# Optimization experiments

Hardware: AMD Instinct MI355X
Metric: run time of the kernel (lower is better)

Reference implementation:

```python
import jax, jax.numpy as jnp
import numpy as np

EPS = 1e-16  # matches PyG softmax denominator epsilon


def setup_inputs() -> dict:
    key = jax.random.key(0)
    k1, k2, k3, k4 = jax.random.split(key, 4)
    N, F, G = 200000, 256, 1024
    x = jax.random.normal(k1, (N, F), dtype=jnp.float32)
    batch = jnp.sort(jax.random.randint(k2, (N,), 0, G, dtype=jnp.int64))
    Wg = jax.random.normal(k3, (F, 1), dtype=jnp.float32) / np.sqrt(F)
    bg = jnp.zeros((1,), dtype=jnp.float32)
    Wn = jax.random.normal(k4, (F, F), dtype=jnp.float32) / np.sqrt(F)
    bn = jnp.zeros((F,), dtype=jnp.float32)
    return {"x": x, "batch": batch, "size": G, "Wg": Wg, "bg": bg, "Wn": Wn, "bn": bn}


def reference(x, batch, size, Wg, bg, Wn, bn):
    # gate scores: [N, 1]
    gate = x @ Wg + bg
    # transformed features: [N, F]
    h = x @ Wn + bn
    # per-graph (segment) softmax over gate, numerically stable
    seg_max = jax.ops.segment_max(gate, batch, num_segments=size)  # [G, 1]
    e = jnp.exp(gate - seg_max[batch])                             # [N, 1]
    seg_sum = jax.ops.segment_sum(e, batch, num_segments=size)     # [G, 1]
    alpha = e / (seg_sum[batch] + EPS)                             # [N, 1]
    # weighted scatter-add: [G, F]
    out = jax.ops.segment_sum(alpha * h, batch, num_segments=size)
    return out
```

## Files before the change

### kernel.cpp

```cpp
#include <hip/hip_runtime.h>
#include <math.h>

#define FDIM 256
#define EPSF 1e-16f
#define K4_ROWS 2

__device__ __forceinline__ float dot4(float4 a, float4 b) {
    return a.x * b.x + a.y * b.y + a.z * b.z + a.w * b.w;
}

__global__ void __launch_bounds__(256) k_ranges(const int* __restrict__ batch,
                                                int* __restrict__ seg_start,
                                                int N, int G) {
    int i = blockIdx.x * blockDim.x + threadIdx.x;
    if (i > N) return;
    int b  = (i == N) ? G : batch[i];
    int bp = (i == 0) ? -1 : batch[i - 1];
    for (int g = bp + 1; g <= b; ++g) seg_start[g] = i;
}

__global__ void __launch_bounds__(256) k_fused(const int* __restrict__ seg_start,
                                               const float* __restrict__ x,
                                               const float* __restrict__ Wg,
                                               float* __restrict__ yp,
                                               float* __restrict__ sp) {
    int b = blockIdx.x;
    int g = b >> 1, half = b & 1;
    int s0 = seg_start[g];
    int e0 = seg_start[g + 1];
    int mid = s0 + ((e0 - s0) >> 1);
    int rs = half ? mid : s0;
    int re = half ? e0 : mid;

    __shared__ float s_s[16];
    __shared__ float s_acc[16][FDIM];

    int wave = threadIdx.x >> 6;
    int group = (threadIdx.x >> 4) & 3;
    int l16 = threadIdx.x & 15;
    int part = (wave << 2) | group;

    const float4 wg0 = *reinterpret_cast<const float4*>(Wg +   0 + l16 * 4);
    const float4 wg1 = *reinterpret_cast<const float4*>(Wg +  64 + l16 * 4);
    const float4 wg2 = *reinterpret_cast<const float4*>(Wg + 128 + l16 * 4);
    const float4 wg3 = *reinterpret_cast<const float4*>(Wg + 192 + l16 * 4);

    float4 a0 = make_float4(0.f, 0.f, 0.f, 0.f);
    float4 a1 = a0, a2 = a0, a3 = a0;
    float s = 0.f;

    int r = rs + part;
    for (; r + 16 < re; r += 32) {
        const float* rp0 = x + (size_t)r * FDIM;
        const float* rp1 = x + (size_t)(r + 16) * FDIM;
        float4 x0 = *reinterpret_cast<const float4*>(rp0 +   0 + l16 * 4);
        float4 x1 = *reinterpret_cast<const float4*>(rp0 +  64 + l16 * 4);
        float4 x2 = *reinterpret_cast<const float4*>(rp0 + 128 + l16 * 4);
        float4 x3 = *reinterpret_cast<const float4*>(rp0 + 192 + l16 * 4);
        float4 y0 = *reinterpret_cast<const float4*>(rp1 +   0 + l16 * 4);
        float4 y1 = *reinterpret_cast<const float4*>(rp1 +  64 + l16 * 4);
        float4 y2 = *reinterpret_cast<const float4*>(rp1 + 128 + l16 * 4);
        float4 y3 = *reinterpret_cast<const float4*>(rp1 + 192 + l16 * 4);
        float d0 = dot4(x0, wg0) + dot4(x1, wg1) + dot4(x2, wg2) + dot4(x3, wg3);
        float d1 = dot4(y0, wg0) + dot4(y1, wg1) + dot4(y2, wg2) + dot4(y3, wg3);
        #pragma unroll
        for (int off = 1; off < 16; off <<= 1) {
            d0 += __shfl_xor(d0, off, 64);
            d1 += __shfl_xor(d1, off, 64);
        }
        float w0 = __expf(d0);
        float w1 = __expf(d1);
        a0.x += w0 * x0.x; a0.y += w0 * x0.y; a0.z += w0 * x0.z; a0.w += w0 * x0.w;
        a1.x += w0 * x1.x; a1.y += w0 * x1.y; a1.z += w0 * x1.z; a1.w += w0 * x1.w;
        a2.x += w0 * x2.x; a2.y += w0 * x2.y; a2.z += w0 * x2.z; a2.w += w0 * x2.w;
        a3.x += w0 * x3.x; a3.y += w0 * x3.y; a3.z += w0 * x3.z; a3.w += w0 * x3.w;
        s += w0;
        a0.x += w1 * y0.x; a0.y += w1 * y0.y; a0.z += w1 * y0.z; a0.w += w1 * y0.w;
        a1.x += w1 * y1.x; a1.y += w1 * y1.y; a1.z += w1 * y1.z; a1.w += w1 * y1.w;
        a2.x += w1 * y2.x; a2.y += w1 * y2.y; a2.z += w1 * y2.z; a2.w += w1 * y2.w;
        a3.x += w1 * y3.x; a3.y += w1 * y3.y; a3.z += w1 * y3.z; a3.w += w1 * y3.w;
        s += w1;
    }
    if (r < re) {
        const float* rp = x + (size_t)r * FDIM;
        float4 x0 = *reinterpret_cast<const float4*>(rp +   0 + l16 * 4);
        float4 x1 = *reinterpret_cast<const float4*>(rp +  64 + l16 * 4);
        float4 x2 = *reinterpret_cast<const float4*>(rp + 128 + l16 * 4);
        float4 x3 = *reinterpret_cast<const float4*>(rp + 192 + l16 * 4);
        float d = dot4(x0, wg0) + dot4(x1, wg1) + dot4(x2, wg2) + dot4(x3, wg3);
        #pragma unroll
        for (int off = 1; off < 16; off <<= 1) d += __shfl_xor(d, off, 64);
        float w = __expf(d);
        a0.x += w * x0.x; a0.y += w * x0.y; a0.z += w * x0.z; a0.w += w * x0.w;
        a1.x += w * x1.x; a1.y += w * x1.y; a1.z += w * x1.z; a1.w += w * x1.w;
        a2.x += w * x2.x; a2.y += w * x2.y; a2.z += w * x2.z; a2.w += w * x2.w;
        a3.x += w * x3.x; a3.y += w * x3.y; a3.z += w * x3.z; a3.w += w * x3.w;
        s += w;
    }

    *reinterpret_cast<float4*>(&s_acc[part][  0 + l16 * 4]) = a0;
    *reinterpret_cast<float4*>(&s_acc[part][ 64 + l16 * 4]) = a1;
    *reinterpret_cast<float4*>(&s_acc[part][128 + l16 * 4]) = a2;
    *reinterpret_cast<float4*>(&s_acc[part][192 + l16 * 4]) = a3;
    if (l16 == 0) s_s[part] = s;
    __syncthreads();

    int c = threadIdx.x;
    float v = 0.f;
    #pragma unroll
    for (int p = 0; p < 16; ++p) v += s_acc[p][c];
    yp[(size_t)b * FDIM + c] = v;
    if (threadIdx.x == 0) {
        float t = 0.f;
        #pragma unroll
        for (int p = 0; p < 16; ++p) t += s_s[p];
        sp[b] = t;
    }
}

__global__ void __launch_bounds__(256) k4_out(const float* __restrict__ yp,
                                              const float* __restrict__ sp,
                                              const float* __restrict__ Wn,
                                              const float* __restrict__ bn,
                                              float* __restrict__ out, int G) {
    int g0 = blockIdx.x * K4_ROWS;
    __shared__ float ys[K4_ROWS][FDIM];
    __shared__ float s_alpha[K4_ROWS];
    int c = threadIdx.x;
    #pragma unroll
    for (int r = 0; r < K4_ROWS; ++r) {
        int g = g0 + r;
        if (g < G) {
            float sg = sp[2 * g] + sp[2 * g + 1];
            float inv = 1.0f / (sg + EPSF);
            ys[r][c] = (yp[(size_t)(2 * g) * FDIM + c] +
                        yp[(size_t)(2 * g + 1) * FDIM + c]) * inv;
            if (c == 0) s_alpha[r] = sg * inv;
        } else {
            ys[r][c] = 0.f;
            if (c == 0) s_alpha[r] = 0.f;
        }
    }
    __syncthreads();
    float acc[K4_ROWS];
    #pragma unroll
    for (int r = 0; r < K4_ROWS; ++r) acc[r] = 0.f;
    #pragma unroll 8
    for (int k = 0; k < FDIM; ++k) {
        float w = Wn[k * FDIM + c];
        #pragma unroll
        for (int r = 0; r < K4_ROWS; ++r) acc[r] += ys[r][k] * w;
    }
    float bv = bn[c];
    #pragma unroll
    for (int r = 0; r < K4_ROWS; ++r) {
        int g = g0 + r;
        if (g < G) out[(size_t)g * FDIM + c] = acc[r] + s_alpha[r] * bv;
    }
}

extern "C" void kernel_launch(void* const* d_in, const int* in_sizes, int n_in,
                              void* d_out, int out_size, void* d_ws, size_t ws_size,
                              hipStream_t stream) {
    const float* x     = (const float*)d_in[0];
    const int*   batch = (const int*)d_in[1];
    const float* Wg    = (const float*)d_in[3];
    const float* Wn    = (const float*)d_in[5];
    const float* bn    = (const float*)d_in[6];
    float* out = (float*)d_out;

    int N = in_sizes[1];
    int G = out_size / FDIM;

    int*   seg_start = (int*)d_ws;
    float* sp = (float*)(seg_start + ((G + 2) & ~1));
    float* yp = sp + 2 * G;

    k_ranges<<<(N + 1 + 255) / 256, 256, 0, stream>>>(batch, seg_start, N, G);
    k_fused<<<2 * G, 256, 0, stream>>>(seg_start, x, Wg, yp, sp);
    k4_out<<<(G + K4_ROWS - 1) / K4_ROWS, 256, 0, stream>>>(yp, sp, Wn, bn, out, G);
}
```

Baseline: 53.60 us.

## Map one row per wave with register prefetch; widen output GEMV blocks

The fused segment kernel now assigns whole 256-float rows to a single wave, so each lane holds one float4. Each wave processes four rows per iteration and prefetches the next four rows into registers while computing the current ones. This shrinks the shared-memory reduction from 16 partials to 4 and replaces the tail branch with predicated loads. The output kernel uses 1024-thread blocks that each handle four graphs, one thread per graph row and column. The cost is a full 64-lane shuffle reduction per row, and 4-row work granularity can leave some waves idle on small segments.

```diff
diff --git a/kernel.cpp b/kernel.cpp
--- a/kernel.cpp
+++ b/kernel.cpp
@@ -3,7 +3,6 @@
 
 #define FDIM 256
 #define EPSF 1e-16f
-#define K4_ROWS 2
 
 __device__ __forceinline__ float dot4(float4 a, float4 b) {
     return a.x * b.x + a.y * b.y + a.z * b.z + a.w * b.w;
@@ -32,131 +31,99 @@
     int rs = half ? mid : s0;
     int re = half ? e0 : mid;
 
-    __shared__ float s_s[16];
-    __shared__ float s_acc[16][FDIM];
+    __shared__ float s_s[4];
+    __shared__ float s_acc[4][FDIM];
 
     int wave = threadIdx.x >> 6;
-    int group = (threadIdx.x >> 4) & 3;
-    int l16 = threadIdx.x & 15;
-    int part = (wave << 2) | group;
+    int lane = threadIdx.x & 63;
+    int c4 = lane * 4;
 
-    const float4 wg0 = *reinterpret_cast<const float4*>(Wg +   0 + l16 * 4);
-    const float4 wg1 = *reinterpret_cast<const float4*>(Wg +  64 + l16 * 4);
-    const float4 wg2 = *reinterpret_cast<const float4*>(Wg + 128 + l16 * 4);
-    const float4 wg3 = *reinterpret_cast<const float4*>(Wg + 192 + l16 * 4);
+    const float4 wgv = *reinterpret_cast<const float4*>(Wg + c4);
+    const float4 zero4 = make_float4(0.f, 0.f, 0.f, 0.f);
 
-    float4 a0 = make_float4(0.f, 0.f, 0.f, 0.f);
-    float4 a1 = a0, a2 = a0, a3 = a0;
+    float4 acc = zero4;
     float s = 0.f;
 
-    int r = rs + part;
-    for (; r + 16 < re; r += 32) {
-        const float* rp0 = x + (size_t)r * FDIM;
-        const float* rp1 = x + (size_t)(r + 16) * FDIM;
-        float4 x0 = *reinterpret_cast<const float4*>(rp0 +   0 + l16 * 4);
-        float4 x1 = *reinterpret_cast<const float4*>(rp0 +  64 + l16 * 4);
-        float4 x2 = *reinterpret_cast<const float4*>(rp0 + 128 + l16 * 4);
-        float4 x3 = *reinterpret_cast<const float4*>(rp0 + 192 + l16 * 4);
-        float4 y0 = *reinterpret_cast<const float4*>(rp1 +   0 + l16 * 4);
-        float4 y1 = *reinterpret_cast<const float4*>(rp1 +  64 + l16 * 4);
-        float4 y2 = *reinterpret_cast<const float4*>(rp1 + 128 + l16 * 4);
-        float4 y3 = *reinterpret_cast<const float4*>(rp1 + 192 + l16 * 4);
-        float d0 = dot4(x0, wg0) + dot4(x1, wg1) + dot4(x2, wg2) + dot4(x3, wg3);
-        float d1 = dot4(y0, wg0) + dot4(y1, wg1) + dot4(y2, wg2) + dot4(y3, wg3);
+#define LOADROW(dst, row) \
+    dst = ((row) < re) ? *reinterpret_cast<const float4*>(x + (size_t)(row) * FDIM + c4) : zero4;
+
+    int base = rs + wave * 4;
+    float4 c0, c1, c2, c3;
+    LOADROW(c0, base); LOADROW(c1, base + 1);
+    LOADROW(c2, base + 2); LOADROW(c3, base + 3);
+
+    for (int r = base; r < re; r += 16) {
+        float4 n0, n1, n2, n3;
+        int nr = r + 16;
+        LOADROW(n0, nr); LOADROW(n1, nr + 1);
+        LOADROW(n2, nr + 2); LOADROW(n3, nr + 3);
+
+        float d0 = dot4(c0, wgv);
+        float d1 = dot4(c1, wgv);
+        float d2 = dot4(c2, wgv);
+        float d3 = dot4(c3, wgv);
         #pragma unroll
-        for (int off = 1; off < 16; off <<= 1) {
+        for (int off = 1; off < 64; off <<= 1) {
             d0 += __shfl_xor(d0, off, 64);
             d1 += __shfl_xor(d1, off, 64);
+            d2 += __shfl_xor(d2, off, 64);
+            d3 += __shfl_xor(d3, off, 64);
         }
         float w0 = __expf(d0);
-        float w1 = __expf(d1);
-        a0.x += w0 * x0.x; a0.y += w0 * x0.y; a0.z += w0 * x0.z; a0.w += w0 * x0.w;
-        a1.x += w0 * x1.x; a1.y += w0 * x1.y; a1.z += w0 * x1.z; a1.w += w0 * x1.w;
-        a2.x += w0 * x2.x; a2.y += w0 * x2.y; a2.z += w0 * x2.z; a2.w += w0 * x2.w;
-        a3.x += w0 * x3.x; a3.y += w0 * x3.y; a3.z += w0 * x3.z; a3.w += w0 * x3.w;
-        s += w0;
-        a0.x += w1 * y0.x; a0.y += w1 * y0.y; a0.z += w1 * y0.z; a0.w += w1 * y0.w;
-        a1.x += w1 * y1.x; a1.y += w1 * y1.y; a1.z += w1 * y1.z; a1.w += w1 * y1.w;
-        a2.x += w1 * y2.x; a2.y += w1 * y2.y; a2.z += w1 * y2.z; a2.w += w1 * y2.w;
-        a3.x += w1 * y3.x; a3.y += w1 * y3.y; a3.z += w1 * y3.z; a3.w += w1 * y3.w;
-        s += w1;
+        float w1 = (r + 1 < re) ? __expf(d1) : 0.f;
+        float w2 = (r + 2 < re) ? __expf(d2) : 0.f;
+        float w3 = (r + 3 < re) ? __expf(d3) : 0.f;
+        acc.x += w0 * c0.x + w1 * c1.x + w2 * c2.x + w3 * c3.x;
+        acc.y += w0 * c0.y + w1 * c1.y + w2 * c2.y + w3 * c3.y;
+        acc.z += w0 * c0.z + w1 * c1.z + w2 * c2.z + w3 * c3.z;
+        acc.w += w0 * c0.w + w1 * c1.w + w2 * c2.w + w3 * c3.w;
+        s += (w0 + w1) + (w2 + w3);
+        c0 = n0; c1 = n1; c2 = n2; c3 = n3;
     }
-    if (r < re) {
-        const float* rp = x + (size_t)r * FDIM;
-        float4 x0 = *reinterpret_cast<const float4*>(rp +   0 + l16 * 4);
-        float4 x1 = *reinterpret_cast<const float4*>(rp +  64 + l16 * 4);
-        float4 x2 = *reinterpret_cast<const float4*>(rp + 128 + l16 * 4);
-        float4 x3 = *reinterpret_cast<const float4*>(rp + 192 + l16 * 4);
-        float d = dot4(x0, wg0) + dot4(x1, wg1) + dot4(x2, wg2) + dot4(x3, wg3);
-        #pragma unroll
-        for (int off = 1; off < 16; off <<= 1) d += __shfl_xor(d, off, 64);
-        float w = __expf(d);
-        a0.x += w * x0.x; a0.y += w * x0.y; a0.z += w * x0.z; a0.w += w * x0.w;
-        a1.x += w * x1.x; a1.y += w * x1.y; a1.z += w * x1.z; a1.w += w * x1.w;
-        a2.x += w * x2.x; a2.y += w * x2.y; a2.z += w * x2.z; a2.w += w * x2.w;
-        a3.x += w * x3.x; a3.y += w * x3.y; a3.z += w * x3.z; a3.w += w * x3.w;
-        s += w;
-    }
+#undef LOADROW
 
-    *reinterpret_cast<float4*>(&s_acc[part][  0 + l16 * 4]) = a0;
-    *reinterpret_cast<float4*>(&s_acc[part][ 64 + l16 * 4]) = a1;
-    *reinterpret_cast<float4*>(&s_acc[part][128 + l16 * 4]) = a2;
-    *reinterpret_cast<float4*>(&s_acc[part][192 + l16 * 4]) = a3;
-    if (l16 == 0) s_s[part] = s;
+    *reinterpret_cast<float4*>(&s_acc[wave][c4]) = acc;
+    if (lane == 0) s_s[wave] = s;
     __syncthreads();
 
     int c = threadIdx.x;
-    float v = 0.f;
-    #pragma unroll
-    for (int p = 0; p < 16; ++p) v += s_acc[p][c];
+    float v = (s_acc[0][c] + s_acc[1][c]) + (s_acc[2][c] + s_acc[3][c]);
     yp[(size_t)b * FDIM + c] = v;
-    if (threadIdx.x == 0) {
-        float t = 0.f;
-        #pragma unroll
-        for (int p = 0; p < 16; ++p) t += s_s[p];
-        sp[b] = t;
-    }
+    if (threadIdx.x == 0)
+        sp[b] = (s_s[0] + s_s[1]) + (s_s[2] + s_s[3]);
 }
 
-__global__ void __launch_bounds__(256) k4_out(const float* __restrict__ yp,
-                                              const float* __restrict__ sp,
-                                              const float* __restrict__ Wn,
-                                              const float* __restrict__ bn,
-                                              float* __restrict__ out, int G) {
-    int g0 = blockIdx.x * K4_ROWS;
-    __shared__ float ys[K4_ROWS][FDIM];
-    __shared__ float s_alpha[K4_ROWS];
-    int c = threadIdx.x;
-    #pragma unroll
-    for (int r = 0; r < K4_ROWS; ++r) {
-        int g = g0 + r;
-        if (g < G) {
-            float sg = sp[2 * g] + sp[2 * g + 1];
-            float inv = 1.0f / (sg + EPSF);
-            ys[r][c] = (yp[(size_t)(2 * g) * FDIM + c] +
-                        yp[(size_t)(2 * g + 1) * FDIM + c]) * inv;
-            if (c == 0) s_alpha[r] = sg * inv;
-        } else {
-            ys[r][c] = 0.f;
-            if (c == 0) s_alpha[r] = 0.f;
-        }
+__global__ void __launch_bounds__(1024) k4_out(const float* __restrict__ yp,
+                                               const float* __restrict__ sp,
+                                               const float* __restrict__ Wn,
+                                               const float* __restrict__ bn,
+                                               float* __restrict__ out, int G) {
+    int g0 = blockIdx.x * 4;
+    int r = threadIdx.x >> 8;
+    int c = threadIdx.x & 255;
+    int g = g0 + r;
+
+    __shared__ float ys[4][FDIM];
+    __shared__ float s_alpha[4];
+
+    float sg = (g < G) ? (sp[2 * g] + sp[2 * g + 1]) : 0.f;
+    float inv = 1.0f / (sg + EPSF);
+    if (g < G) {
+        ys[r][c] = (yp[(size_t)(2 * g) * FDIM + c] +
+                    yp[(size_t)(2 * g + 1) * FDIM + c]) * inv;
+        if (c == 0) s_alpha[r] = sg * inv;
+    } else {
+        ys[r][c] = 0.f;
+        if (c == 0) s_alpha[r] = 0.f;
     }
     __syncthreads();
-    float acc[K4_ROWS];
-    #pragma unroll
-    for (int r = 0; r < K4_ROWS; ++r) acc[r] = 0.f;
+
+    float acc = 0.f;
     #pragma unroll 8
-    for (int k = 0; k < FDIM; ++k) {
-        float w = Wn[k * FDIM + c];
-        #pragma unroll
-        for (int r = 0; r < K4_ROWS; ++r) acc[r] += ys[r][k] * w;
-    }
-    float bv = bn[c];
-    #pragma unroll
-    for (int r = 0; r < K4_ROWS; ++r) {
-        int g = g0 + r;
-        if (g < G) out[(size_t)g * FDIM + c] = acc[r] + s_alpha[r] * bv;
-    }
+    for (int k = 0; k < FDIM; ++k)
+        acc += ys[r][k] * Wn[k * FDIM + c];
+
+    if (g < G) out[(size_t)g * FDIM + c] = acc + s_alpha[r] * bn[c];
 }
 
 extern "C" void kernel_launch(void* const* d_in, const int* in_sizes, int n_in,
@@ -178,5 +145,5 @@
 
     k_ranges<<<(N + 1 + 255) / 256, 256, 0, stream>>>(batch, seg_start, N, G);
     k_fused<<<2 * G, 256, 0, stream>>>(seg_start, x, Wg, yp, sp);
-    k4_out<<<(G + K4_ROWS - 1) / K4_ROWS, 256, 0, stream>>>(yp, sp, Wn, bn, out, G);
+    k4_out<<<(G + 3) / 4, 1024, 0, stream>>>(yp, sp, Wn, bn, out, G);
 }
```

Measured after the change: 56.34 us. +5.1%, slower.
